# Performance work log

Measured on AMD Instinct MI355X. Metric: run time of the kernel, lower is better.

The kernel has to match this reference:

```python
import jax, jax.numpy as jnp
import numpy as np

N_NODES = 50000
N_RELS = 50
N_CLASSES = 40
EMB_DIM = 16
RP = 16
N_TRIPLES = 400000


def setup_inputs() -> dict:
    rng = np.random.default_rng(0)
    s = rng.integers(0, N_NODES, size=N_TRIPLES)
    r = rng.integers(0, N_RELS, size=N_TRIPLES)
    o = rng.integers(0, N_NODES, size=N_TRIPLES)
    # unique (s,o) pairs, as in torch.unique(pairs, dim=0, return_inverse=True)
    pairs = np.stack([s, o], axis=1)
    unique_pairs, inverse = np.unique(pairs, axis=0, return_inverse=True)
    nt = unique_pairs.shape[0]
    # relation_matrix COO (nt, num_rels), coalesced (duplicate (row,col) summed)
    keys = inverse.astype(np.int64) * N_RELS + r
    uk, counts = np.unique(keys, return_counts=True)
    rm_rows = (uk // N_RELS).astype(np.int32)
    rm_cols = (uk % N_RELS).astype(np.int32)
    rm_vals = counts.astype(np.float32)
    # hindices / vindices exactly as in __init__ (note o*rm / s*rm construction)
    s_u = unique_pairs[:, 0].astype(np.int64)
    o_u = unique_pairs[:, 1].astype(np.int64)
    rm = np.arange(RP, dtype=np.int64)[:, None]            # (rp, 1)
    h_rows = np.broadcast_to(s_u[None, :], (RP, nt)).reshape(-1).astype(np.int32)
    h_cols = (o_u[None, :] * rm).reshape(-1).astype(np.int32)
    v_rows = (s_u[None, :] * rm).reshape(-1).astype(np.int32)
    v_cols = np.broadcast_to(o_u[None, :], (RP, nt)).reshape(-1).astype(np.int32)
    # float params (xavier-like scale for weights, randn for rel emb, zero biases)
    key = jax.random.key(0)
    k1, k2, k3 = jax.random.split(key, 3)
    gain = np.sqrt(2.0)  # relu gain
    w1_std = gain * np.sqrt(2.0 / (N_NODES + EMB_DIM))
    w2_std = gain * np.sqrt(2.0 / (EMB_DIM + N_CLASSES))
    return {
        'rel_emb': jax.random.normal(k1, (N_RELS, RP), dtype=jnp.float32),
        'weights1': jax.random.normal(k2, (RP, N_NODES, EMB_DIM), dtype=jnp.float32) * w1_std,
        'weights2': jax.random.normal(k3, (RP, EMB_DIM, N_CLASSES), dtype=jnp.float32) * w2_std,
        'bias1': jnp.zeros((EMB_DIM,), dtype=jnp.float32),
        'bias2': jnp.zeros((N_CLASSES,), dtype=jnp.float32),
        'rm_rows': jnp.asarray(rm_rows),
        'rm_cols': jnp.asarray(rm_cols),
        'rm_vals': jnp.asarray(rm_vals),
        'h_rows': jnp.asarray(h_rows),
        'h_cols': jnp.asarray(h_cols),
        'v_rows': jnp.asarray(v_rows),
        'v_cols': jnp.asarray(v_cols),
    }


def reference(rel_emb, weights1, weights2, bias1, bias2,
              rm_rows, rm_cols, rm_vals, h_rows, h_cols, v_rows, v_cols):
    rp, n, e = weights1.shape
    nt = h_rows.shape[0] // rp
    # latents = sparse.mm(relation_matrix, relation_embeddings) -> (nt, rp)
    latents = jax.ops.segment_sum(rm_vals[:, None] * rel_emb[rm_cols], rm_rows,
                                  num_segments=nt)
    latents = jax.nn.softmax(latents, axis=1)
    lf = latents.T.reshape(-1)                              # (rp*nt,)
    # sum_sparse(hindices, lf, (n, n*rp), row=False): per-column sums, gathered
    colsum = jax.ops.segment_sum(lf, h_cols, num_segments=n * rp)
    ln = lf / colsum[h_cols]
    # spmm(hindices, ln, (n, n*rp), weights1_flat) -> (n, e)
    w1f = weights1.reshape(rp * n, e)
    h = jax.ops.segment_sum(ln[:, None] * w1f[h_cols], h_rows, num_segments=n)
    h = jax.nn.relu(h + bias1)
    # sum_sparse(vindices, lf, (n*rp, n), row=True): per-row sums, gathered
    rowsum = jax.ops.segment_sum(lf, v_rows, num_segments=n * rp)
    ln2 = lf / rowsum[v_rows]
    # spmm(vindices, ln2, (n*rp, n), h) -> (n*rp, e)
    h2 = jax.ops.segment_sum(ln2[:, None] * h[v_cols], v_rows, num_segments=n * rp)
    h2 = h2.reshape(rp, n, e)
    out = jnp.einsum('rhc,rnh->nc', weights2, h2) + bias2
    return out
```

## Files before the change

### kernel.cpp

```cpp
#include <hip/hip_runtime.h>

#define RP 16
#define EMB 16
#define NC 40

__global__ void k_count(const int* __restrict__ s_u, const int* __restrict__ o_u,
                        int* __restrict__ cnt_s, int* __restrict__ cnt_o, int nt) {
    int t = blockIdx.x * blockDim.x + threadIdx.x;
    if (t < nt) {
        atomicAdd(&cnt_s[s_u[t]], 1);
        atomicAdd(&cnt_o[o_u[t]], 1);
    }
}

__global__ void k_scan_blk(const int* __restrict__ cnt_s, int* __restrict__ offs_s,
                           const int* __restrict__ cnt_o, int* __restrict__ offs_o,
                           int* __restrict__ partials, int n, int nblk) {
    const int* in = blockIdx.y ? cnt_o : cnt_s;
    int* out = blockIdx.y ? offs_o : offs_s;
    int tid = threadIdx.x;
    int i0 = blockIdx.x * 1024 + tid * 4;
    int v[4];
    #pragma unroll
    for (int q = 0; q < 4; ++q) {
        int i = i0 + q;
        v[q] = (i < n) ? in[i] : 0;
    }
    int tsum = v[0] + v[1] + v[2] + v[3];
    int lane = tid & 63, wid = tid >> 6;
    int x = tsum;
    #pragma unroll
    for (int d = 1; d < 64; d <<= 1) {
        int u = __shfl_up(x, d, 64);
        if (lane >= d) x += u;
    }
    __shared__ int wsum[4];
    if (lane == 63) wsum[wid] = x;
    __syncthreads();
    int woff = 0;
    for (int wq = 0; wq < wid; ++wq) woff += wsum[wq];
    int run = woff + x - tsum;
    #pragma unroll
    for (int q = 0; q < 4; ++q) {
        int i = i0 + q;
        if (i < n) out[i] = run;
        run += v[q];
    }
    if (tid == 255) partials[blockIdx.y * nblk + blockIdx.x] = run;
}

__global__ void k_scan_top(int* __restrict__ partials, int nblk) {
    int w = threadIdx.x >> 6;
    int lane = threadIdx.x & 63;
    int carry = 0;
    for (int base = 0; base < nblk; base += 64) {
        int idx = base + lane;
        int v = (idx < nblk) ? partials[w * nblk + idx] : 0;
        int x = v;
        #pragma unroll
        for (int d = 1; d < 64; d <<= 1) {
            int u = __shfl_up(x, d, 64);
            if (lane >= d) x += u;
        }
        if (idx < nblk) partials[w * nblk + idx] = carry + x - v;
        carry += __shfl(x, 63, 64);
    }
}

__global__ void k_scan_add(int* __restrict__ offs_s, int* __restrict__ cur_s,
                           int* __restrict__ offs_o, int* __restrict__ cur_o,
                           const int* __restrict__ partials, int n, int nblk) {
    int* out = blockIdx.y ? offs_o : offs_s;
    int* cur = blockIdx.y ? cur_o : cur_s;
    int add = partials[blockIdx.y * nblk + blockIdx.x];
    int i0 = blockIdx.x * 1024 + threadIdx.x * 4;
    #pragma unroll
    for (int q = 0; q < 4; ++q) {
        int i = i0 + q;
        if (i < n) {
            int vv = out[i] + add;
            out[i] = vv;
            cur[i] = vv;
        }
    }
}

__global__ void k_latents(const float* __restrict__ rel_emb,
                          const int* __restrict__ rows,
                          const int* __restrict__ cols,
                          const float* __restrict__ vals,
                          const int* __restrict__ s_u,
                          const int* __restrict__ o_u,
                          int* __restrict__ cur_s, int* __restrict__ cur_o,
                          float* __restrict__ lat_s, float* __restrict__ lat_o,
                          int* __restrict__ ou_s, int* __restrict__ su_o,
                          int nm) {
    int i = blockIdx.x * blockDim.x + threadIdx.x;
    int e = i >> 4, k = i & 15;
    if (e >= nm) return;
    int row = rows[e];
    if (e > 0 && rows[e - 1] == row) return;
    float acc = vals[e] * rel_emb[cols[e] * RP + k];
    while (e + 1 < nm && rows[e + 1] == row) {
        ++e;
        acc += vals[e] * rel_emb[cols[e] * RP + k];
    }
    float m = acc;
    #pragma unroll
    for (int d = 1; d < 16; d <<= 1) m = fmaxf(m, __shfl_xor(m, d, 16));
    float v = expf(acc - m);
    float s = v;
    #pragma unroll
    for (int d = 1; d < 16; d <<= 1) s += __shfl_xor(s, d, 16);
    v = v / s;
    int ps = 0, po = 0, su = 0, ou = 0;
    if (k == 0) {
        su = s_u[row];
        ou = o_u[row];
        ps = atomicAdd(&cur_s[su], 1);
        po = atomicAdd(&cur_o[ou], 1);
    }
    ps = __shfl(ps, 0, 16);
    po = __shfl(po, 0, 16);
    lat_s[(size_t)ps * RP + k] = v;
    lat_o[(size_t)po * RP + k] = v;
    if (k == 0) {
        ou_s[ps] = ou;
        su_o[po] = su;
    }
}

__global__ void k_r0(const float* __restrict__ lat_s,
                     float* __restrict__ rowsum, float* __restrict__ colsum,
                     int nt) {
    float acc = 0.f;
    for (int t = blockIdx.x * blockDim.x + threadIdx.x; t < nt;
         t += gridDim.x * blockDim.x)
        acc += lat_s[(size_t)t * RP];
    #pragma unroll
    for (int d = 32; d; d >>= 1) acc += __shfl_down(acc, d, 64);
    __shared__ float sm[4];
    int lane = threadIdx.x & 63, wid = threadIdx.x >> 6;
    if (lane == 0) sm[wid] = acc;
    __syncthreads();
    if (threadIdx.x == 0) {
        float tot = sm[0] + sm[1] + sm[2] + sm[3];
        atomicAdd(&rowsum[0], tot);
        atomicAdd(&colsum[0], tot);
    }
}

__global__ void k_latsum(const float* __restrict__ lat_s,
                         const int* __restrict__ offs_s,
                         const int* __restrict__ cnt_s,
                         float* __restrict__ rowsum,
                         const float* __restrict__ lat_o,
                         const int* __restrict__ offs_o,
                         const int* __restrict__ cnt_o,
                         float* __restrict__ colsum, int n) {
    const float* lat = blockIdx.y ? lat_o : lat_s;
    const int* offs = blockIdx.y ? offs_o : offs_s;
    const int* cnt  = blockIdx.y ? cnt_o : cnt_s;
    float* dst      = blockIdx.y ? colsum : rowsum;
    int i = blockIdx.x * blockDim.x + threadIdx.x;
    int v = i >> 4, k = i & 15;
    if (v >= n) return;
    int beg = offs[v], d = cnt[v];
    if (d == 0) return;
    float ls = 0.f;
    int j = 0;
    for (; j + 4 <= d; j += 4) {
        float a0 = lat[(size_t)(beg + j + 0) * RP + k];
        float a1 = lat[(size_t)(beg + j + 1) * RP + k];
        float a2 = lat[(size_t)(beg + j + 2) * RP + k];
        float a3 = lat[(size_t)(beg + j + 3) * RP + k];
        ls += (a0 + a1) + (a2 + a3);
    }
    for (; j < d; ++j) ls += lat[(size_t)(beg + j) * RP + k];
    if (k >= 1) atomicAdd(&dst[v * k], ls);
}

__global__ void k_h_acc(const float* __restrict__ lat_o,
                        const int* __restrict__ offs_o,
                        const int* __restrict__ cnt_o,
                        const int* __restrict__ su_o,
                        const float* __restrict__ colsum,
                        const float* __restrict__ w1,
                        float* __restrict__ h, int n) {
    int i = blockIdx.x * blockDim.x + threadIdx.x;
    int o = i >> 4, k = i & 15;
    if (o >= n) return;
    int d = cnt_o[o];
    if (d == 0) return;
    int beg = offs_o[o];
    float W[RP];
    #pragma unroll
    for (int r = 0; r < RP; ++r)
        W[r] = w1[(size_t)(o * r) * EMB + k];
    float rcp_cs = 1.f / colsum[o * k];
    for (int j = 0; j < d; ++j) {
        float ln = lat_o[(size_t)(beg + j) * RP + k] * rcp_cs;
        int s = su_o[beg + j];
        float acc = 0.f;
        #pragma unroll
        for (int r = 0; r < RP; ++r)
            acc += __shfl(ln, r, 16) * W[r];
        atomicAdd(&h[s * EMB + k], acc);
    }
}

__global__ void k_h2(const float* __restrict__ lat_s,
                     const int* __restrict__ offs_s,
                     const int* __restrict__ cnt_s,
                     const int* __restrict__ ou_s,
                     const float* __restrict__ rowsum,
                     const float* __restrict__ h,
                     const float* __restrict__ bias1,
                     float* __restrict__ h2,
                     float* __restrict__ r0part, int n) {
    __shared__ float r0acc[EMB];
    if (threadIdx.x < EMB) r0acc[threadIdx.x] = 0.f;
    __syncthreads();
    int i = blockIdx.x * blockDim.x + threadIdx.x;
    int s = i >> 4, k = i & 15;
    float b1k = bias1[k];
    float M[RP];
    #pragma unroll
    for (int r = 0; r < RP; ++r) M[r] = 0.f;
    int d = 0;
    if (s < n) {
        int beg = offs_s[s];
        d = cnt_s[s];
        for (int j = 0; j < d; ++j) {
            int o = ou_s[beg + j];
            float hv = fmaxf(h[o * EMB + k] + b1k, 0.f);
            float lat = lat_s[(size_t)(beg + j) * RP + k];
            #pragma unroll
            for (int r = 0; r < RP; ++r)
                M[r] += __shfl(lat, r, 16) * hv;
        }
    }
    if (s < n && d > 0) {
        float rs = rowsum[s * k];
        float rs0 = __shfl(rs, 0, 16);
        atomicAdd(&r0acc[k], M[0] / rs0);
        #pragma unroll
        for (int r = 1; r < RP; ++r) {
            float rsr = __shfl(rs, r, 16);
            atomicAdd(&h2[(size_t)(s * r) * EMB + k], M[r] / rsr);
        }
    }
    __syncthreads();
    if (threadIdx.x < EMB)
        r0part[(size_t)blockIdx.x * EMB + threadIdx.x] = r0acc[threadIdx.x];
}

__global__ void k_h2r0(const float* __restrict__ r0part,
                       float* __restrict__ h2, int nblk) {
    __shared__ float red[1024];
    int k = threadIdx.x & 15, j0 = threadIdx.x >> 4;
    float acc = 0.f;
    for (int j = j0; j < nblk; j += 64)
        acc += r0part[(size_t)j * EMB + k];
    red[j0 * 16 + k] = acc;
    __syncthreads();
    #pragma unroll
    for (int st = 32; st >= 1; st >>= 1) {
        if (j0 < st) red[j0 * 16 + k] += red[(j0 + st) * 16 + k];
        __syncthreads();
    }
    if (threadIdx.x < 16) h2[threadIdx.x] += red[threadIdx.x];
}

#define CB2 20
__global__ void k_out(const float* __restrict__ w2,
                      const float* __restrict__ bias2,
                      const float* __restrict__ h2,
                      float* __restrict__ out, int n) {
    __shared__ float w2s[RP * EMB * NC];
    for (int i = threadIdx.x; i < RP * EMB * NC; i += 256)
        w2s[i] = w2[i];
    __syncthreads();
    int gi = blockIdx.x * blockDim.x + threadIdx.x;
    int node = gi >> 1;
    int c0 = (gi & 1) * CB2;
    if (node >= n) return;
    float acc[CB2];
    #pragma unroll
    for (int c = 0; c < CB2; ++c) acc[c] = bias2[c0 + c];
    for (int rq = 0; rq < RP; ++rq) {
        const float4* h2row = (const float4*)&h2[((size_t)rq * n + node) * EMB];
        float4 hv4[4];
        #pragma unroll
        for (int q = 0; q < 4; ++q) hv4[q] = h2row[q];
        const float* hv = (const float*)hv4;
        #pragma unroll
        for (int hh = 0; hh < EMB; ++hh) {
            const float4* wrow = (const float4*)&w2s[(rq * EMB + hh) * NC + c0];
            float hvv = hv[hh];
            #pragma unroll
            for (int q5 = 0; q5 < 5; ++q5) {
                float4 wv = wrow[q5];
                acc[q5 * 4 + 0] += wv.x * hvv;
                acc[q5 * 4 + 1] += wv.y * hvv;
                acc[q5 * 4 + 2] += wv.z * hvv;
                acc[q5 * 4 + 3] += wv.w * hvv;
            }
        }
    }
    float4* op = (float4*)&out[node * NC + c0];
    #pragma unroll
    for (int q5 = 0; q5 < 5; ++q5)
        op[q5] = make_float4(acc[q5 * 4], acc[q5 * 4 + 1],
                             acc[q5 * 4 + 2], acc[q5 * 4 + 3]);
}

extern "C" void kernel_launch(void* const* d_in, const int* in_sizes, int n_in,
                              void* d_out, int out_size, void* d_ws, size_t ws_size,
                              hipStream_t stream) {
    const float* rel_emb = (const float*)d_in[0];
    const float* w1      = (const float*)d_in[1];
    const float* w2      = (const float*)d_in[2];
    const float* b1      = (const float*)d_in[3];
    const float* b2      = (const float*)d_in[4];
    const int*   rm_rows = (const int*)d_in[5];
    const int*   rm_cols = (const int*)d_in[6];
    const float* rm_vals = (const float*)d_in[7];
    const int*   h_rows  = (const int*)d_in[8];
    const int*   v_cols  = (const int*)d_in[11];

    const int nm = in_sizes[5];
    const int ne = in_sizes[8];
    const int nt = ne / RP;
    const int n  = in_sizes[1] / (RP * EMB);

    const int B = 256;
    const int nblk_h2 = (n * 16 + B - 1) / B;
    const int nblk_sc = (n + 1023) / 1024;

    char* w = (char*)d_ws;
    float* colsum = (float*)w;  w += (size_t)n * RP * 4;
    float* rowsum = (float*)w;  w += (size_t)n * RP * 4;
    float* h2     = (float*)w;  w += (size_t)n * RP * EMB * 4;
    float* h      = (float*)w;  w += (size_t)n * EMB * 4;
    int* cnt_s    = (int*)w;    w += (size_t)n * 4;
    int* cnt_o    = (int*)w;    w += (size_t)n * 4;
    size_t zero_bytes = (size_t)(w - (char*)d_ws);
    float* lat_s  = (float*)w;  w += (size_t)nt * RP * 4;
    float* lat_o  = (float*)w;  w += (size_t)nt * RP * 4;
    int* ou_s     = (int*)w;    w += (size_t)nt * 4;
    int* su_o     = (int*)w;    w += (size_t)nt * 4;
    int* offs_s   = (int*)w;    w += (size_t)n * 4;
    int* cur_s    = (int*)w;    w += (size_t)n * 4;
    int* offs_o   = (int*)w;    w += (size_t)n * 4;
    int* cur_o    = (int*)w;    w += (size_t)n * 4;
    float* r0part = (float*)w;  w += (size_t)nblk_h2 * EMB * 4;
    int* partials = (int*)w;    w += (size_t)2 * nblk_sc * 4;
    if ((size_t)(w - (char*)d_ws) > ws_size) return;

    hipMemsetAsync(d_ws, 0, zero_bytes, stream);

    k_count<<<dim3((nt + B - 1) / B), dim3(B), 0, stream>>>(
        h_rows, v_cols, cnt_s, cnt_o, nt);
    k_scan_blk<<<dim3(nblk_sc, 2), dim3(B), 0, stream>>>(
        cnt_s, offs_s, cnt_o, offs_o, partials, n, nblk_sc);
    k_scan_top<<<dim3(1), dim3(128), 0, stream>>>(partials, nblk_sc);
    k_scan_add<<<dim3(nblk_sc, 2), dim3(B), 0, stream>>>(
        offs_s, cur_s, offs_o, cur_o, partials, n, nblk_sc);
    k_latents<<<dim3((nm * 16 + B - 1) / B), dim3(B), 0, stream>>>(
        rel_emb, rm_rows, rm_cols, rm_vals, h_rows, v_cols,
        cur_s, cur_o, lat_s, lat_o, ou_s, su_o, nm);
    k_r0<<<dim3(64), dim3(B), 0, stream>>>(lat_s, rowsum, colsum, nt);
    k_latsum<<<dim3((n * 16 + B - 1) / B, 2), dim3(B), 0, stream>>>(
        lat_s, offs_s, cnt_s, rowsum, lat_o, offs_o, cnt_o, colsum, n);
    k_h_acc<<<dim3((n * 16 + B - 1) / B), dim3(B), 0, stream>>>(
        lat_o, offs_o, cnt_o, su_o, colsum, w1, h, n);
    k_h2<<<dim3(nblk_h2), dim3(B), 0, stream>>>(
        lat_s, offs_s, cnt_s, ou_s, rowsum, h, b1, h2, r0part, n);
    k_h2r0<<<dim3(1), dim3(1024), 0, stream>>>(r0part, h2, nblk_h2);
    k_out<<<dim3((n * 2 + B - 1) / B), dim3(B), 0, stream>>>(
        w2, b2, h2, (float*)d_out, n);
}
```

Baseline: 305.2 us.

## Use subject-sorted triple order directly and fold row normalization into later kernels

Since unique pairs are already sorted by subject, latents are written in triple order (lat_t) and used directly as the subject-CSR layout. This drops the cur_s atomic scatter, the ou_s index array and the subject half of k_latsum. Row sums are now accumulated inside k_h2, and the division by rowsum is deferred to k_out, which multiplies h2 by a reciprocal. The approach depends on the triples arriving sorted by subject and adds per-element rowsum atomics in k_h2.

```diff
diff --git a/kernel.cpp b/kernel.cpp
--- a/kernel.cpp
+++ b/kernel.cpp
@@ -91,9 +91,9 @@
                           const float* __restrict__ vals,
                           const int* __restrict__ s_u,
                           const int* __restrict__ o_u,
-                          int* __restrict__ cur_s, int* __restrict__ cur_o,
-                          float* __restrict__ lat_s, float* __restrict__ lat_o,
-                          int* __restrict__ ou_s, int* __restrict__ su_o,
+                          int* __restrict__ cur_o,
+                          float* __restrict__ lat_t, float* __restrict__ lat_o,
+                          float* __restrict__ lat0, int* __restrict__ su_o,
                           int nm) {
     int i = blockIdx.x * blockDim.x + threadIdx.x;
     int e = i >> 4, k = i & 15;
@@ -113,30 +113,25 @@
     #pragma unroll
     for (int d = 1; d < 16; d <<= 1) s += __shfl_xor(s, d, 16);
     v = v / s;
-    int ps = 0, po = 0, su = 0, ou = 0;
+    lat_t[(size_t)row * RP + k] = v;
+    int po = 0;
     if (k == 0) {
-        su = s_u[row];
-        ou = o_u[row];
-        ps = atomicAdd(&cur_s[su], 1);
+        int ou = o_u[row];
         po = atomicAdd(&cur_o[ou], 1);
-    }
-    ps = __shfl(ps, 0, 16);
+        su_o[po] = s_u[row];
+        lat0[row] = v;
+    }
     po = __shfl(po, 0, 16);
-    lat_s[(size_t)ps * RP + k] = v;
     lat_o[(size_t)po * RP + k] = v;
-    if (k == 0) {
-        ou_s[ps] = ou;
-        su_o[po] = su;
-    }
-}
-
-__global__ void k_r0(const float* __restrict__ lat_s,
+}
+
+__global__ void k_r0(const float* __restrict__ lat0,
                      float* __restrict__ rowsum, float* __restrict__ colsum,
                      int nt) {
     float acc = 0.f;
     for (int t = blockIdx.x * blockDim.x + threadIdx.x; t < nt;
          t += gridDim.x * blockDim.x)
-        acc += lat_s[(size_t)t * RP];
+        acc += lat0[t];
     #pragma unroll
     for (int d = 32; d; d >>= 1) acc += __shfl_down(acc, d, 64);
     __shared__ float sm[4];
@@ -150,34 +145,26 @@
     }
 }
 
-__global__ void k_latsum(const float* __restrict__ lat_s,
-                         const int* __restrict__ offs_s,
-                         const int* __restrict__ cnt_s,
-                         float* __restrict__ rowsum,
-                         const float* __restrict__ lat_o,
+__global__ void k_latsum(const float* __restrict__ lat_o,
                          const int* __restrict__ offs_o,
                          const int* __restrict__ cnt_o,
                          float* __restrict__ colsum, int n) {
-    const float* lat = blockIdx.y ? lat_o : lat_s;
-    const int* offs = blockIdx.y ? offs_o : offs_s;
-    const int* cnt  = blockIdx.y ? cnt_o : cnt_s;
-    float* dst      = blockIdx.y ? colsum : rowsum;
     int i = blockIdx.x * blockDim.x + threadIdx.x;
     int v = i >> 4, k = i & 15;
     if (v >= n) return;
-    int beg = offs[v], d = cnt[v];
+    int beg = offs_o[v], d = cnt_o[v];
     if (d == 0) return;
     float ls = 0.f;
     int j = 0;
     for (; j + 4 <= d; j += 4) {
-        float a0 = lat[(size_t)(beg + j + 0) * RP + k];
-        float a1 = lat[(size_t)(beg + j + 1) * RP + k];
-        float a2 = lat[(size_t)(beg + j + 2) * RP + k];
-        float a3 = lat[(size_t)(beg + j + 3) * RP + k];
+        float a0 = lat_o[(size_t)(beg + j + 0) * RP + k];
+        float a1 = lat_o[(size_t)(beg + j + 1) * RP + k];
+        float a2 = lat_o[(size_t)(beg + j + 2) * RP + k];
+        float a3 = lat_o[(size_t)(beg + j + 3) * RP + k];
         ls += (a0 + a1) + (a2 + a3);
     }
-    for (; j < d; ++j) ls += lat[(size_t)(beg + j) * RP + k];
-    if (k >= 1) atomicAdd(&dst[v * k], ls);
+    for (; j < d; ++j) ls += lat_o[(size_t)(beg + j) * RP + k];
+    if (k >= 1) atomicAdd(&colsum[(size_t)v * k], ls);
 }
 
 __global__ void k_h_acc(const float* __restrict__ lat_o,
@@ -197,7 +184,7 @@
     #pragma unroll
     for (int r = 0; r < RP; ++r)
         W[r] = w1[(size_t)(o * r) * EMB + k];
-    float rcp_cs = 1.f / colsum[o * k];
+    float rcp_cs = 1.f / colsum[(size_t)o * k];
     for (int j = 0; j < d; ++j) {
         float ln = lat_o[(size_t)(beg + j) * RP + k] * rcp_cs;
         int s = su_o[beg + j];
@@ -209,11 +196,11 @@
     }
 }
 
-__global__ void k_h2(const float* __restrict__ lat_s,
+__global__ void k_h2(const float* __restrict__ lat_t,
                      const int* __restrict__ offs_s,
                      const int* __restrict__ cnt_s,
-                     const int* __restrict__ ou_s,
-                     const float* __restrict__ rowsum,
+                     const int* __restrict__ o_u,
+                     float* __restrict__ rowsum,
                      const float* __restrict__ h,
                      const float* __restrict__ bias1,
                      float* __restrict__ h2,
@@ -227,28 +214,27 @@
     float M[RP];
     #pragma unroll
     for (int r = 0; r < RP; ++r) M[r] = 0.f;
+    float rs_acc = 0.f;
     int d = 0;
     if (s < n) {
         int beg = offs_s[s];
         d = cnt_s[s];
         for (int j = 0; j < d; ++j) {
-            int o = ou_s[beg + j];
+            int o = o_u[beg + j];
             float hv = fmaxf(h[o * EMB + k] + b1k, 0.f);
-            float lat = lat_s[(size_t)(beg + j) * RP + k];
+            float lat = lat_t[(size_t)(beg + j) * RP + k];
+            rs_acc += lat;
             #pragma unroll
             for (int r = 0; r < RP; ++r)
                 M[r] += __shfl(lat, r, 16) * hv;
         }
     }
     if (s < n && d > 0) {
-        float rs = rowsum[s * k];
-        float rs0 = __shfl(rs, 0, 16);
-        atomicAdd(&r0acc[k], M[0] / rs0);
-        #pragma unroll
-        for (int r = 1; r < RP; ++r) {
-            float rsr = __shfl(rs, r, 16);
-            atomicAdd(&h2[(size_t)(s * r) * EMB + k], M[r] / rsr);
-        }
+        if (k >= 1) atomicAdd(&rowsum[(size_t)s * k], rs_acc);
+        atomicAdd(&r0acc[k], M[0]);
+        #pragma unroll
+        for (int r = 1; r < RP; ++r)
+            atomicAdd(&h2[(size_t)(s * r) * EMB + k], M[r]);
     }
     __syncthreads();
     if (threadIdx.x < EMB)
@@ -276,6 +262,7 @@
 __global__ void k_out(const float* __restrict__ w2,
                       const float* __restrict__ bias2,
                       const float* __restrict__ h2,
+                      const float* __restrict__ rowsum,
                       float* __restrict__ out, int n) {
     __shared__ float w2s[RP * EMB * NC];
     for (int i = threadIdx.x; i < RP * EMB * NC; i += 256)
@@ -289,7 +276,10 @@
     #pragma unroll
     for (int c = 0; c < CB2; ++c) acc[c] = bias2[c0 + c];
     for (int rq = 0; rq < RP; ++rq) {
-        const float4* h2row = (const float4*)&h2[((size_t)rq * n + node) * EMB];
+        size_t flat = (size_t)rq * n + node;
+        float rs = rowsum[flat];
+        float rcp = (rs != 0.f) ? 1.f / rs : 0.f;
+        const float4* h2row = (const float4*)&h2[flat * EMB];
         float4 hv4[4];
         #pragma unroll
         for (int q = 0; q < 4; ++q) hv4[q] = h2row[q];
@@ -297,7 +287,7 @@
         #pragma unroll
         for (int hh = 0; hh < EMB; ++hh) {
             const float4* wrow = (const float4*)&w2s[(rq * EMB + hh) * NC + c0];
-            float hvv = hv[hh];
+            float hvv = hv[hh] * rcp;
             #pragma unroll
             for (int q5 = 0; q5 < 5; ++q5) {
                 float4 wv = wrow[q5];
@@ -346,9 +336,9 @@
     int* cnt_s    = (int*)w;    w += (size_t)n * 4;
     int* cnt_o    = (int*)w;    w += (size_t)n * 4;
     size_t zero_bytes = (size_t)(w - (char*)d_ws);
-    float* lat_s  = (float*)w;  w += (size_t)nt * RP * 4;
+    float* lat_t  = (float*)w;  w += (size_t)nt * RP * 4;
     float* lat_o  = (float*)w;  w += (size_t)nt * RP * 4;
-    int* ou_s     = (int*)w;    w += (size_t)nt * 4;
+    float* lat0   = (float*)w;  w += (size_t)nt * 4;
     int* su_o     = (int*)w;    w += (size_t)nt * 4;
     int* offs_s   = (int*)w;    w += (size_t)n * 4;
     int* cur_s    = (int*)w;    w += (size_t)n * 4;
@@ -369,15 +359,15 @@
         offs_s, cur_s, offs_o, cur_o, partials, n, nblk_sc);
     k_latents<<<dim3((nm * 16 + B - 1) / B), dim3(B), 0, stream>>>(
         rel_emb, rm_rows, rm_cols, rm_vals, h_rows, v_cols,
-        cur_s, cur_o, lat_s, lat_o, ou_s, su_o, nm);
-    k_r0<<<dim3(64), dim3(B), 0, stream>>>(lat_s, rowsum, colsum, nt);
-    k_latsum<<<dim3((n * 16 + B - 1) / B, 2), dim3(B), 0, stream>>>(
-        lat_s, offs_s, cnt_s, rowsum, lat_o, offs_o, cnt_o, colsum, n);
+        cur_o, lat_t, lat_o, lat0, su_o, nm);
+    k_r0<<<dim3(64), dim3(B), 0, stream>>>(lat0, rowsum, colsum, nt);
+    k_latsum<<<dim3((n * 16 + B - 1) / B), dim3(B), 0, stream>>>(
+        lat_o, offs_o, cnt_o, colsum, n);
     k_h_acc<<<dim3((n * 16 + B - 1) / B), dim3(B), 0, stream>>>(
         lat_o, offs_o, cnt_o, su_o, colsum, w1, h, n);
     k_h2<<<dim3(nblk_h2), dim3(B), 0, stream>>>(
-        lat_s, offs_s, cnt_s, ou_s, rowsum, h, b1, h2, r0part, n);
+        lat_t, offs_s, cnt_s, v_cols, rowsum, h, b1, h2, r0part, n);
     k_h2r0<<<dim3(1), dim3(1024), 0, stream>>>(r0part, h2, nblk_h2);
     k_out<<<dim3((n * 2 + B - 1) / B), dim3(B), 0, stream>>>(
-        w2, b2, h2, (float*)d_out, n);
-}
+        w2, b2, h2, rowsum, (float*)d_out, n);
+}
```

After: 280.5 us. -8.1%, faster.
